# Kernel tuning notes

Hardware: AMD Instinct MI355X
Metric: run time of the kernel (lower is better)

The kernel has to match this reference:

```python
import jax, jax.numpy as jnp
import numpy as np
from jax import lax

N = 131072
E = 2097152
D = 128
B = 16
NC = 5
EPS = 1e-5


def setup_inputs() -> dict:
    key = jax.random.key(0)
    ks = jax.random.split(key, 32)
    inp = {
        'h': jax.random.normal(ks[0], (N, D), jnp.float32),
        'edge_w': jax.random.uniform(ks[1], (E,), jnp.float32),
        'src': jax.random.randint(ks[2], (E,), 0, N),
        'dst': jax.random.randint(ks[3], (E,), 0, N),
        'node_gid': jnp.sort(jax.random.randint(ks[4], (N,), 0, B)),
        'num_graphs': B,
    }
    s = 0.05
    inp['conv1_w'] = jax.random.normal(ks[5], (D, D, 3), jnp.float32) * s
    inp['conv1_b'] = jax.random.normal(ks[6], (D,), jnp.float32) * s
    inp['conv2_w'] = jax.random.normal(ks[7], (D, D, 3), jnp.float32) * s
    inp['conv2_b'] = jax.random.normal(ks[8], (D,), jnp.float32) * s
    inp['conv3_w'] = jax.random.normal(ks[9], (D, D, 3), jnp.float32) * s
    inp['conv3_b'] = jax.random.normal(ks[10], (D,), jnp.float32) * s
    inp['press_w'] = jax.random.normal(ks[11], (1, 3, 3), jnp.float32) * s
    inp['press_b'] = jax.random.normal(ks[12], (1,), jnp.float32) * s
    names = ['g11', 'g12', 'g13', 'g2', 'g3', 'g4']
    for i, nm in enumerate(names):
        inp[nm + '_w'] = jax.random.normal(ks[13 + 2 * i], (D, D), jnp.float32) * s
        inp[nm + '_b'] = jax.random.normal(ks[14 + 2 * i], (D,), jnp.float32) * s
    inp['bn_g'] = jnp.ones((D,), jnp.float32)
    inp['bn_b'] = jnp.zeros((D,), jnp.float32)
    inp['cls1_w'] = jax.random.normal(ks[25], (D, 3 * D), jnp.float32) * s
    inp['cls1_b'] = jax.random.normal(ks[26], (D,), jnp.float32) * s
    inp['cls2_w'] = jax.random.normal(ks[27], (NC, D), jnp.float32) * s
    inp['cls2_b'] = jax.random.normal(ks[28], (NC,), jnp.float32) * s
    return inp


def _conv1d_nodes(x, w, b, dil, pad):
    # x: [N, D] treated as a length-N 1D signal with D channels (as in original)
    y = lax.conv_general_dilated(x.T[None], w, window_strides=(1,),
                                 padding=[(pad, pad)], rhs_dilation=(dil,),
                                 dimension_numbers=('NCH', 'OIH', 'NCH'))
    return (y[0] + b[:, None]).T  # [N, D]


def _bn(x, g, b):
    mu = jnp.mean(x, axis=0)
    var = jnp.mean((x - mu) ** 2, axis=0)
    return (x - mu) * lax.rsqrt(var + EPS) * g + b


def _gconv(h, W, b, src, dst, ew, n):
    # DGL GraphConv norm='none': aggregate-first (in==out), msg = h[src]*ew, sum at dst, then @W + b
    msg = h[src] * ew[:, None]            # [E, D]
    agg = jax.ops.segment_sum(msg, dst, num_segments=n)
    return agg @ W + b


def reference(h, edge_w, src, dst, node_gid, num_graphs,
              conv1_w, conv1_b, conv2_w, conv2_b, conv3_w, conv3_b,
              press_w, press_b,
              g11_w, g11_b, g12_w, g12_b, g13_w, g13_b,
              g2_w, g2_b, g3_w, g3_b, g4_w, g4_b,
              bn_g, bn_b, cls1_w, cls1_b, cls2_w, cls2_b):
    n = h.shape[0]
    c1 = _conv1d_nodes(h, conv1_w, conv1_b, 1, 1)
    c2 = _conv1d_nodes(h, conv2_w, conv2_b, 2, 2)
    c3 = _conv1d_nodes(h, conv3_w, conv3_b, 3, 3)
    h01 = _bn(jax.nn.relu(c1) + c2, bn_g, bn_b)
    h02 = _bn(jax.nn.relu(c2) + c3, bn_g, bn_b)
    h03 = _bn(jax.nn.relu(c3) + c1, bn_g, bn_b)

    a1 = jax.nn.relu(_gconv(h01, g11_w, g11_b, src, dst, edge_w, n))
    a2 = jax.nn.relu(_gconv(h02, g12_w, g12_b, src, dst, edge_w, n))
    a3 = jax.nn.relu(_gconv(h03, g13_w, g13_b, src, dst, edge_w, n))
    stacked = jnp.stack([a1, a2, a3], axis=1)  # [N, 3, D]
    pressed = lax.conv_general_dilated(stacked, press_w, window_strides=(1,),
                                       padding=[(1, 1)],
                                       dimension_numbers=('NCH', 'OIH', 'NCH'))
    ac_h1 = pressed[:, 0, :] + press_b  # [N, D]
    ac_h1 = _bn(ac_h1, bn_g, bn_b)      # dropout is identity in eval

    ac_h2 = jax.nn.relu(_gconv(ac_h1, g2_w, g2_b, src, dst, edge_w, n))
    ac_h3 = jax.nn.relu(_gconv(ac_h2, g3_w, g3_b, src, dst, edge_w, n))
    ac_h4 = jax.nn.relu(_gconv(ac_h3, g4_w, g4_b, src, dst, edge_w, n))

    hg2 = jax.ops.segment_sum(ac_h2, node_gid, num_segments=num_graphs)
    hg3 = jax.ops.segment_sum(ac_h3, node_gid, num_segments=num_graphs)
    hg4 = jax.ops.segment_sum(ac_h4, node_gid, num_segments=num_graphs)
    hg = jnp.concatenate([hg2, hg3, hg4], axis=1)  # [B, 3D]
    out = (hg @ cls1_w.T + cls1_b) @ cls2_w.T + cls2_b  # [B, NC]
    return out
```

## Files before the change

kernel.cpp:

```cpp
#include <hip/hip_runtime.h>

#define NN 131072
#define NE 2097152

typedef unsigned short u16;
typedef unsigned int u32;
typedef __attribute__((ext_vector_type(8))) short bf16x8;
typedef __attribute__((ext_vector_type(4))) float f32x4;
typedef __attribute__((ext_vector_type(2))) float f32x2;

__device__ __forceinline__ float bf2f(u16 v) {
  unsigned u = ((unsigned)v) << 16;
  return __builtin_bit_cast(float, u);
}
__device__ __forceinline__ float blo(u32 v) {
  return __builtin_bit_cast(float, v << 16);
}
__device__ __forceinline__ float bhi(u32 v) {
  return __builtin_bit_cast(float, v & 0xffff0000u);
}
__device__ __forceinline__ u16 f2bf(float f) {
  unsigned u = __builtin_bit_cast(unsigned, f);
  unsigned r = (u + 0x7fffu + ((u >> 16) & 1u)) >> 16;
  return (u16)r;
}

#define WDQ 3.0518509475997192e-05f

#define H16_OFF 0ull
#define A_OFF 33554432ull
#define B_OFF 67108864ull
#define C_OFF 100663296ull
#define Z_OFF 134217728ull
#define RE_OFF 150994944ull
#define CSR_OFF 167772160ull
#define RP_OFF 184549376ull
#define DEG_OFF 185077760ull
#define SW_OFF 185602048ull
#define BS_OFF 186126336ull
#define SUMS_OFF 186130432ull
#define HG_OFF 186134528ull
#define WT16_OFF 186159104ull
#define WP16_OFF 186472448ull
#define CP_OFF 186681344ull
#define SV_OFF 186683392ull
#define SHV_OFF 186685440ull

__global__ void zerok(int* __restrict__ deg, float* __restrict__ sums,
                      float* __restrict__ hg) {
  int i = blockIdx.x * 256 + threadIdx.x;
  deg[i] = 0;
  if (i < 1024) sums[i] = 0.f;
  if (i < 6144) hg[i] = 0.f;
}

__global__ void h2bf(const float* __restrict__ h, u16* __restrict__ o) {
  int i = blockIdx.x * 256 + threadIdx.x;
  float4 v0 = *(const float4*)(h + (size_t)i * 8);
  float4 v1 = *(const float4*)(h + (size_t)i * 8 + 4);
  ushort4 a, b;
  a.x = f2bf(v0.x); a.y = f2bf(v0.y); a.z = f2bf(v0.z); a.w = f2bf(v0.w);
  b.x = f2bf(v1.x); b.y = f2bf(v1.y); b.z = f2bf(v1.z); b.w = f2bf(v1.w);
  *(ushort4*)(o + (size_t)i * 8) = a;
  *(ushort4*)(o + (size_t)i * 8 + 4) = b;
}

__global__ void prep_wT16(const float* __restrict__ w1, const float* __restrict__ w2,
                          const float* __restrict__ w3, u16* __restrict__ wT) {
  int e = blockIdx.x * 256 + threadIdx.x;
  if (e >= 3 * 3 * 128 * 128) return;
  int o = e & 127;
  int i = (e >> 7) & 127;
  int ct = e >> 14;
  int t = ct % 3, c = ct / 3;
  const float* w = (c == 0) ? w1 : (c == 1) ? w2 : w3;
  wT[(size_t)(c * 3 + t) * 17408 + o * 136 + i] = f2bf(w[(o * 128 + i) * 3 + t]);
}

__global__ void wprep16(const float* __restrict__ W, const float* __restrict__ sv,
                        u16* __restrict__ Wt) {
  int e = blockIdx.x * 256 + threadIdx.x;
  int o = e & 127, i = e >> 7;
  float s = sv ? sv[i] : 1.f;
  Wt[o * 136 + i] = f2bf(s * W[i * 128 + o]);
}

__global__ void cprep(const float* __restrict__ W, const float* __restrict__ shv,
                      float* __restrict__ cp) {
  int j = threadIdx.x;
  float a = 0.f;
  for (int i = 0; i < 128; ++i) a += shv[i] * W[i * 128 + j];
  cp[j] = a;
}

__global__ void bnparam(const float* __restrict__ sums, const float* __restrict__ g,
                        const float* __restrict__ b, float* __restrict__ sv,
                        float* __restrict__ shv, int tensor0) {
  int t = tensor0 + blockIdx.x;
  int o = threadIdx.x;
  float mu = sums[t * 256 + o] / (float)NN;
  float var = sums[t * 256 + 128 + o] / (float)NN - mu * mu;
  float s = g[o] * rsqrtf(var + 1e-5f);
  sv[t * 128 + o] = s;
  shv[t * 128 + o] = b[o] - mu * s;
}

template <int TAPS, int DIL, int OUT8>
__global__ __launch_bounds__(256, 4) void mfma_gemm(const u16* __restrict__ x,
                                                    const u16* __restrict__ wt,
                                                    u16* __restrict__ z) {
  __shared__ u16 sh[17408];
  int tid = threadIdx.x;
  int lane = tid & 63, wave = tid >> 6;
  int n0 = blockIdx.x * 128;
  int m = lane & 15, quad = lane >> 4;
  int koff = quad * 8;
  f32x4 acc[2][8];
#pragma unroll
  for (int a = 0; a < 2; ++a)
#pragma unroll
    for (int b = 0; b < 8; ++b) acc[a][b] = (f32x4){0.f, 0.f, 0.f, 0.f};
  int rbase = n0 + wave * 32 + m;

  for (int t = 0; t < TAPS; ++t) {
    if (TAPS > 1) __syncthreads();
    for (int idx = tid; idx < 2176; idx += 256)
      ((uint4*)sh)[idx] = ((const uint4*)(wt + (size_t)t * 17408))[idx];
    __syncthreads();
    const int shift = (TAPS == 3) ? (t - 1) * DIL : 0;
#pragma unroll
    for (int ks = 0; ks < 4; ++ks) {
      bf16x8 af[2];
#pragma unroll
      for (int rt = 0; rt < 2; ++rt) {
        int row = rbase + rt * 16 + shift;
        if (TAPS == 3) {
          int rc = min(max(row, 0), NN - 1);
          bf16x8 v = *(const bf16x8*)(x + (size_t)rc * 128 + ks * 32 + koff);
          bf16x8 zz = {};
          af[rt] = (row >= 0 && row < NN) ? v : zz;
        } else {
          af[rt] = *(const bf16x8*)(x + (size_t)row * 128 + ks * 32 + koff);
        }
      }
#pragma unroll
      for (int ct = 0; ct < 8; ++ct) {
        bf16x8 bf = *(const bf16x8*)(sh + (ct * 16 + m) * 136 + ks * 32 + koff);
        acc[0][ct] =
            __builtin_amdgcn_mfma_f32_16x16x32_bf16(af[0], bf, acc[0][ct], 0, 0, 0);
        acc[1][ct] =
            __builtin_amdgcn_mfma_f32_16x16x32_bf16(af[1], bf, acc[1][ct], 0, 0, 0);
      }
    }
  }
  __syncthreads();
#pragma unroll
  for (int rt = 0; rt < 2; ++rt)
#pragma unroll
    for (int ct = 0; ct < 8; ++ct)
#pragma unroll
      for (int r = 0; r < 4; ++r) {
        int rowl = wave * 32 + rt * 16 + quad * 4 + r;
        sh[rowl * 136 + ct * 16 + m] = f2bf(acc[rt][ct][r]);
      }
  __syncthreads();
  if (OUT8) {
    unsigned char* z8 = (unsigned char*)z;
#pragma unroll
    for (int it = 0; it < 8; ++it) {
      int q = tid + it * 256;
      int row = q >> 4, g = q & 15;
      uint4 v = *(const uint4*)(sh + row * 136 + g * 8);
      int w0 = __builtin_amdgcn_cvt_pk_fp8_f32(blo(v.x), bhi(v.x), 0, false);
      w0 = __builtin_amdgcn_cvt_pk_fp8_f32(blo(v.y), bhi(v.y), w0, true);
      int w1 = __builtin_amdgcn_cvt_pk_fp8_f32(blo(v.z), bhi(v.z), 0, false);
      w1 = __builtin_amdgcn_cvt_pk_fp8_f32(blo(v.w), bhi(v.w), w1, true);
      uint2 st;
      st.x = (u32)w0;
      st.y = (u32)w1;
      *(uint2*)(z8 + (size_t)(n0 + row) * 128 + g * 8) = st;
    }
  } else {
#pragma unroll
    for (int it = 0; it < 8; ++it) {
      int q = tid + it * 256;
      int row = q >> 4, g = q & 15;
      uint4 v = *(const uint4*)(sh + row * 136 + g * 8);
      *(uint4*)(z + (size_t)(n0 + row) * 128 + g * 8) = v;
    }
  }
}

__global__ __launch_bounds__(256) void combine(u16* __restrict__ A, u16* __restrict__ B,
                                               u16* __restrict__ C,
                                               const float* __restrict__ b1,
                                               const float* __restrict__ b2,
                                               const float* __restrict__ b3,
                                               float* __restrict__ sums) {
  __shared__ float red[2 * 128 * 6];
  int tid = threadIdx.x;
  int o = tid & 127, half = tid >> 7;
  int n0 = blockIdx.x * 32 + half * 16;
  float bb1 = b1[o], bb2 = b2[o], bb3 = b3[o];
  float s1 = 0, q1 = 0, s2 = 0, q2 = 0, s3 = 0, q3 = 0;
  for (int j = 0; j < 16; ++j) {
    size_t idx = (size_t)(n0 + j) * 128 + o;
    float c1 = bf2f(A[idx]) + bb1, c2 = bf2f(B[idx]) + bb2, c3 = bf2f(C[idx]) + bb3;
    float v1 = fmaxf(c1, 0.f) + c2;
    float v2 = fmaxf(c2, 0.f) + c3;
    float v3 = fmaxf(c3, 0.f) + c1;
    A[idx] = f2bf(v1);
    B[idx] = f2bf(v2);
    C[idx] = f2bf(v3);
    s1 += v1; q1 += v1 * v1;
    s2 += v2; q2 += v2 * v2;
    s3 += v3; q3 += v3 * v3;
  }
  int ri = (half * 128 + o) * 6;
  red[ri + 0] = s1; red[ri + 1] = q1; red[ri + 2] = s2;
  red[ri + 3] = q2; red[ri + 4] = s3; red[ri + 5] = q3;
  __syncthreads();
  if (half == 0) {
    int rj = (128 + o) * 6;
    atomicAdd(&sums[0 * 256 + o], s1 + red[rj + 0]);
    atomicAdd(&sums[0 * 256 + 128 + o], q1 + red[rj + 1]);
    atomicAdd(&sums[1 * 256 + o], s2 + red[rj + 2]);
    atomicAdd(&sums[1 * 256 + 128 + o], q2 + red[rj + 3]);
    atomicAdd(&sums[2 * 256 + o], s3 + red[rj + 4]);
    atomicAdd(&sums[2 * 256 + 128 + o], q3 + red[rj + 5]);
  }
}

__global__ void deg_rank_k(const int* __restrict__ dst, int* __restrict__ deg,
                           u16* __restrict__ re) {
  int e = blockIdx.x * 256 + threadIdx.x;
  if (e < NE) {
    int d = dst[e];
    int r = atomicAdd(&deg[d], 1);
    re[e] = (u16)r;
  }
}

__global__ void scan1(const int* __restrict__ deg, int* __restrict__ rp,
                      int* __restrict__ bs) {
  __shared__ int s[256];
  int t = threadIdx.x;
  int i = blockIdx.x * 256 + t;
  int v = deg[i];
  s[t] = v;
  for (int off = 1; off < 256; off <<= 1) {
    __syncthreads();
    int x = (t >= off) ? s[t - off] : 0;
    __syncthreads();
    s[t] += x;
  }
  rp[i] = s[t] - v;
  if (t == 255) bs[blockIdx.x] = s[255];
}

__global__ void scan2(int* __restrict__ bs) {
  __shared__ int s[512];
  int t = threadIdx.x;
  int v = bs[t];
  s[t] = v;
  for (int off = 1; off < 512; off <<= 1) {
    __syncthreads();
    int x = (t >= off) ? s[t - off] : 0;
    __syncthreads();
    s[t] += x;
  }
  bs[t] = s[t] - v;
}

__global__ void scan3(int* __restrict__ rp, const int* __restrict__ bs) {
  int i = blockIdx.x * 256 + threadIdx.x;
  rp[i] = rp[i] + bs[blockIdx.x];
  if (i == 0) rp[NN] = NE;
}

__global__ void csr_fill2(const int* __restrict__ src, const int* __restrict__ dst,
                          const float* __restrict__ ew, const int* __restrict__ rp,
                          const u16* __restrict__ re, u32* __restrict__ csrP) {
  int e = blockIdx.x * 256 + threadIdx.x;
  if (e < NE) {
    int d = dst[e];
    int p = rp[d] + (int)re[e];
    u32 q = (u32)(ew[e] * 32767.f + 0.5f);
    csrP[p] = (u32)src[e] | (q << 17);
  }
}

#define AB3 4
__global__ __launch_bounds__(256, 4) void agg3_press(
    const unsigned char* __restrict__ z1, const unsigned char* __restrict__ z2,
    const unsigned char* __restrict__ z3, const u32* __restrict__ csrP,
    const int* __restrict__ rp,
    const float* __restrict__ cp, const float* __restrict__ b1,
    const float* __restrict__ b2, const float* __restrict__ b3,
    const float* __restrict__ pw, const float* __restrict__ pb,
    u16* __restrict__ P, float* __restrict__ sums) {
  __shared__ u16 otile[4][16 * 128];
  __shared__ int ls_rp[4][17];
  int lane = threadIdx.x & 63, wave = threadIdx.x >> 6;
  int d0 = blockIdx.x * 64 + wave * 16;
  if (lane < 17) ls_rp[wave][lane] = rp[d0 + lane];
  float c1x = cp[lane * 2], c1y = cp[lane * 2 + 1];
  float c2x = cp[128 + lane * 2], c2y = cp[128 + lane * 2 + 1];
  float c3x = cp[256 + lane * 2], c3y = cp[256 + lane * 2 + 1];
  float b1x = b1[lane * 2], b1y = b1[lane * 2 + 1];
  float b2x = b2[lane * 2], b2y = b2[lane * 2 + 1];
  float b3x = b3[lane * 2], b3y = b3[lane * 2 + 1];
  float w10 = pw[0], w11 = pw[1], w12 = pw[2];
  float w20 = pw[3], w21 = pw[4], w22 = pw[5];
  float w30 = pw[6], w31 = pw[7], w32 = pw[8];
  float pbv = pb[0];
  __syncthreads();
  int s0 = __builtin_amdgcn_readfirstlane(ls_rp[wave][0]);
  int e0 = __builtin_amdgcn_readfirstlane(ls_rp[wave][16]);
  u32 vob = (u32)(lane * 2);
  float ax1 = 0.f, ay1 = 0.f, ax2 = 0.f, ay2 = 0.f, ax3 = 0.f, ay3 = 0.f;
  float wsum = 0.f;
  float sx = 0.f, qx = 0.f, sy = 0.f, qy = 0.f;
  int ld = 0;
  int nb = __builtin_amdgcn_readfirstlane(ls_rp[wave][1]);

  auto flush = [&]() {
    float swd = wsum;
    float a1x = fmaxf(ax1 + c1x * swd + b1x, 0.f);
    float a1y = fmaxf(ay1 + c1y * swd + b1y, 0.f);
    float a2x = fmaxf(ax2 + c2x * swd + b2x, 0.f);
    float a2y = fmaxf(ay2 + c2y * swd + b2y, 0.f);
    float a3x = fmaxf(ax3 + c3x * swd + b3x, 0.f);
    float a3y = fmaxf(ay3 + c3y * swd + b3y, 0.f);
    float l1 = __shfl_up(a1y, 1); if (lane == 0) l1 = 0.f;
    float l2 = __shfl_up(a2y, 1); if (lane == 0) l2 = 0.f;
    float l3 = __shfl_up(a3y, 1); if (lane == 0) l3 = 0.f;
    float r1 = __shfl_down(a1x, 1); if (lane == 63) r1 = 0.f;
    float r2 = __shfl_down(a2x, 1); if (lane == 63) r2 = 0.f;
    float r3 = __shfl_down(a3x, 1); if (lane == 63) r3 = 0.f;
    float ox = w10 * l1 + w11 * a1x + w12 * a1y + w20 * l2 + w21 * a2x +
               w22 * a2y + w30 * l3 + w31 * a3x + w32 * a3y + pbv;
    float oy = w10 * a1x + w11 * a1y + w12 * r1 + w20 * a2x + w21 * a2y +
               w22 * r2 + w30 * a3x + w31 * a3y + w32 * r3 + pbv;
    u32 pk2 = ((u32)f2bf(oy) << 16) | (u32)f2bf(ox);
    *(u32*)&otile[wave][ld * 128 + lane * 2] = pk2;
    sx += ox; qx += ox * ox;
    sy += oy; qy += oy * oy;
    ax1 = ay1 = ax2 = ay2 = ax3 = ay3 = 0.f;
    wsum = 0.f;
    ++ld;
    nb = __builtin_amdgcn_readfirstlane(ls_rp[wave][ld < 16 ? ld + 1 : 16]);
  };

  if (s0 < e0) {
    int e0m1 = e0 - 1;
    u32 pkA[AB3], pkB[AB3];
    u32 vaA[AB3], vbA[AB3], vcA[AB3], vaB[AB3], vbB[AB3], vcB[AB3];
    float wvA[AB3], wvB[AB3];

#define LOADPK3(PK, J0)                               \
  _Pragma("unroll") for (int k = 0; k < AB3; ++k) {   \
    int jc = (J0) + k;                                \
    jc = jc < e0 ? jc : e0m1;                         \
    PK[k] = csrP[jc];                                 \
  }
#define ISSUE3(VA, VB, VC, WV, PK)                    \
  _Pragma("unroll") for (int k = 0; k < AB3; ++k) {   \
    u32 p = PK[k];                                    \
    u32 off = ((p & 0x1FFFFu) << 7) | vob;            \
    VA[k] = *(const u16*)(z1 + off);                  \
    VB[k] = *(const u16*)(z2 + off);                  \
    VC[k] = *(const u16*)(z3 + off);                  \
    WV[k] = (float)(p >> 17) * WDQ;                   \
  }
#define CONS3(VA, VB, VC, WV, J0)                     \
  _Pragma("unroll") for (int k = 0; k < AB3; ++k) {   \
    int j = (J0) + k;                                 \
    if (j < e0) {                                     \
      while (j >= nb) flush();                        \
      float w = WV[k];                                \
      wsum += w;                                      \
      f32x2 d1 = __builtin_amdgcn_cvt_pk_f32_fp8((int)VA[k], false); \
      f32x2 d2 = __builtin_amdgcn_cvt_pk_f32_fp8((int)VB[k], false); \
      f32x2 d3 = __builtin_amdgcn_cvt_pk_f32_fp8((int)VC[k], false); \
      ax1 += d1.x * w; ay1 += d1.y * w;               \
      ax2 += d2.x * w; ay2 += d2.y * w;               \
      ax3 += d3.x * w; ay3 += d3.y * w;               \
    }                                                 \
  }

    LOADPK3(pkA, s0)
    ISSUE3(vaA, vbA, vcA, wvA, pkA)
    LOADPK3(pkA, s0 + AB3)
    int jb = s0;
    while (true) {
      LOADPK3(pkB, jb + 2 * AB3)
      if (jb + AB3 < e0) { ISSUE3(vaB, vbB, vcB, wvB, pkA) }
      CONS3(vaA, vbA, vcA, wvA, jb)
      if (jb + AB3 >= e0) break;
      LOADPK3(pkA, jb + 3 * AB3)
      if (jb + 2 * AB3 < e0) { ISSUE3(vaA, vbA, vcA, wvA, pkB) }
      CONS3(vaB, vbB, vcB, wvB, jb + AB3)
      if (jb + 2 * AB3 >= e0) break;
      jb += 2 * AB3;
    }
#undef LOADPK3
#undef ISSUE3
#undef CONS3
  }
  while (ld < 16) flush();

  {
    const u16* srcl = &otile[wave][0];
    u16* dstg = P + (size_t)d0 * 128;
#pragma unroll
    for (int i = 0; i < 4; ++i) {
      uint4 v = *(const uint4*)(srcl + i * 512 + lane * 8);
      *(uint4*)(dstg + i * 512 + lane * 8) = v;
    }
  }
  __syncthreads();
  float* red = (float*)&otile[0][0];
  int base = wave * 256 + lane * 4;
  red[base] = sx; red[base + 1] = qx; red[base + 2] = sy; red[base + 3] = qy;
  __syncthreads();
  int t = threadIdx.x;
  if (t < 64) {
    float s0_ = 0, q0_ = 0, s1_ = 0, q1_ = 0;
#pragma unroll
    for (int w = 0; w < 4; ++w) {
      int rb = w * 256 + t * 4;
      s0_ += red[rb]; q0_ += red[rb + 1]; s1_ += red[rb + 2]; q1_ += red[rb + 3];
    }
    atomicAdd(&sums[768 + t * 2], s0_);
    atomicAdd(&sums[768 + 128 + t * 2], q0_);
    atomicAdd(&sums[768 + t * 2 + 1], s1_);
    atomicAdd(&sums[768 + 128 + t * 2 + 1], q1_);
  }
}

#define AB2 8
__global__ __launch_bounds__(256, 4) void agg2(const unsigned char* __restrict__ z,
                                               const u32* __restrict__ csrP,
                                               const int* __restrict__ rp,
                                               const float* __restrict__ cvec,
                                               const float* __restrict__ bvec,
                                               u16* __restrict__ out,
                                               const int* __restrict__ gid,
                                               float* __restrict__ hg, int coloff) {
  __shared__ u16 otile[4][16 * 128];
  __shared__ int ls_rp[4][17];
  __shared__ int ls_gid[4][16];
  int lane = threadIdx.x & 63, wave = threadIdx.x >> 6;
  int d0 = blockIdx.x * 64 + wave * 16;
  if (lane < 17) ls_rp[wave][lane] = rp[d0 + lane];
  if (lane < 16) ls_gid[wave][lane] = gid[d0 + lane];
  float bx = bvec[lane * 2], by = bvec[lane * 2 + 1];
  float cx = cvec ? cvec[lane * 2] : 0.f;
  float cy = cvec ? cvec[lane * 2 + 1] : 0.f;
  __syncthreads();
  int s0 = __builtin_amdgcn_readfirstlane(ls_rp[wave][0]);
  int e0 = __builtin_amdgcn_readfirstlane(ls_rp[wave][16]);
  u32 vob = (u32)(lane * 2);
  float ax = 0.f, ay = 0.f, wsum = 0.f;
  int ld = 0;
  int nb = __builtin_amdgcn_readfirstlane(ls_rp[wave][1]);

  auto flush = [&]() {
    float rx = fmaxf(ax + cx * wsum + bx, 0.f);
    float ry = fmaxf(ay + cy * wsum + by, 0.f);
    u32 pk2 = ((u32)f2bf(ry) << 16) | (u32)f2bf(rx);
    *(u32*)&otile[wave][ld * 128 + lane * 2] = pk2;
    ax = 0.f;
    ay = 0.f;
    wsum = 0.f;
    ++ld;
    nb = __builtin_amdgcn_readfirstlane(ls_rp[wave][ld < 16 ? ld + 1 : 16]);
  };

  if (s0 < e0) {
    int e0m1 = e0 - 1;
    u32 pkA[AB2], pkB[AB2];
    u32 vaA[AB2], vaB[AB2];
    float wvA[AB2], wvB[AB2];

#define LOADPK1(PK, J0)                               \
  _Pragma("unroll") for (int k = 0; k < AB2; ++k) {   \
    int jc = (J0) + k;                                \
    jc = jc < e0 ? jc : e0m1;                         \
    PK[k] = csrP[jc];                                 \
  }
#define ISSUE1(VA, WV, PK)                            \
  _Pragma("unroll") for (int k = 0; k < AB2; ++k) {   \
    u32 p = PK[k];                                    \
    u32 off = ((p & 0x1FFFFu) << 7) | vob;            \
    VA[k] = *(const u16*)(z + off);                   \
    WV[k] = (float)(p >> 17) * WDQ;                   \
  }
#define CONS1(VA, WV, J0)                             \
  _Pragma("unroll") for (int k = 0; k < AB2; ++k) {   \
    int j = (J0) + k;                                 \
    if (j < e0) {                                     \
      while (j >= nb) flush();                        \
      float w = WV[k];                                \
      wsum += w;                                      \
      f32x2 d = __builtin_amdgcn_cvt_pk_f32_fp8((int)VA[k], false); \
      ax += d.x * w;                                  \
      ay += d.y * w;                                  \
    }                                                 \
  }

    LOADPK1(pkA, s0)
    ISSUE1(vaA, wvA, pkA)
    LOADPK1(pkA, s0 + AB2)
    int jb = s0;
    while (true) {
      LOADPK1(pkB, jb + 2 * AB2)
      if (jb + AB2 < e0) { ISSUE1(vaB, wvB, pkA) }
      CONS1(vaA, wvA, jb)
      if (jb + AB2 >= e0) break;
      LOADPK1(pkA, jb + 3 * AB2)
      if (jb + 2 * AB2 < e0) { ISSUE1(vaA, wvA, pkB) }
      CONS1(vaB, wvB, jb + AB2)
      if (jb + 2 * AB2 >= e0) break;
      jb += 2 * AB2;
    }
#undef LOADPK1
#undef ISSUE1
#undef CONS1
  }
  while (ld < 16) flush();

  {
    const u16* srcl = &otile[wave][0];
    u16* dstg = out + (size_t)d0 * 128;
#pragma unroll
    for (int i = 0; i < 4; ++i) {
      uint4 v = *(const uint4*)(srcl + i * 512 + lane * 8);
      *(uint4*)(dstg + i * 512 + lane * 8) = v;
    }
  }
  {
    float runx = 0.f, runy = 0.f;
    int curg = __builtin_amdgcn_readfirstlane(ls_gid[wave][0]);
    for (int r = 0; r < 16; ++r) {
      u32 v = *(const u32*)&otile[wave][r * 128 + lane * 2];
      float rx = blo(v), ry = bhi(v);
      int gn = __builtin_amdgcn_readfirstlane(ls_gid[wave][r]);
      if (gn != curg) {
        atomicAdd(&hg[curg * 384 + coloff + lane * 2], runx);
        atomicAdd(&hg[curg * 384 + coloff + lane * 2 + 1], runy);
        runx = 0.f;
        runy = 0.f;
        curg = gn;
      }
      runx += rx;
      runy += ry;
    }
    atomicAdd(&hg[curg * 384 + coloff + lane * 2], runx);
    atomicAdd(&hg[curg * 384 + coloff + lane * 2 + 1], runy);
  }
}

__global__ void classifier(const float* __restrict__ hg, const float* __restrict__ w1,
                           const float* __restrict__ b1, const float* __restrict__ w2,
                           const float* __restrict__ b2, float* __restrict__ out) {
  __shared__ float sh_hg[16 * 384];
  __shared__ float sh_z[16 * 128];
  int t = threadIdx.x;
  for (int u = t; u < 16 * 384; u += 256) sh_hg[u] = hg[u];
  __syncthreads();
  for (int u = 0; u < 8; ++u) {
    int idx = t + u * 256;
    int b = idx >> 7, o = idx & 127;
    float a = b1[o];
    for (int i = 0; i < 384; ++i) a += sh_hg[b * 384 + i] * w1[o * 384 + i];
    sh_z[b * 128 + o] = a;
  }
  __syncthreads();
  if (t < 80) {
    int b = t / 5, c = t % 5;
    float a = b2[c];
    for (int i = 0; i < 128; ++i) a += sh_z[b * 128 + i] * w2[c * 128 + i];
    out[b * 5 + c] = a;
  }
}

extern "C" void kernel_launch(void* const* d_in, const int* in_sizes, int n_in,
                              void* d_out, int out_size, void* d_ws, size_t ws_size,
                              hipStream_t stream) {
  const float* h = (const float*)d_in[0];
  const float* edge_w = (const float*)d_in[1];
  const int* src = (const int*)d_in[2];
  const int* dst = (const int*)d_in[3];
  const int* gid = (const int*)d_in[4];
  const float* c1w = (const float*)d_in[6];
  const float* c1b = (const float*)d_in[7];
  const float* c2w = (const float*)d_in[8];
  const float* c2b = (const float*)d_in[9];
  const float* c3w = (const float*)d_in[10];
  const float* c3b = (const float*)d_in[11];
  const float* pw = (const float*)d_in[12];
  const float* pb = (const float*)d_in[13];
  const float* g11w = (const float*)d_in[14];
  const float* g11b = (const float*)d_in[15];
  const float* g12w = (const float*)d_in[16];
  const float* g12b = (const float*)d_in[17];
  const float* g13w = (const float*)d_in[18];
  const float* g13b = (const float*)d_in[19];
  const float* g2w = (const float*)d_in[20];
  const float* g2b = (const float*)d_in[21];
  const float* g3w = (const float*)d_in[22];
  const float* g3b = (const float*)d_in[23];
  const float* g4w = (const float*)d_in[24];
  const float* g4b = (const float*)d_in[25];
  const float* bng = (const float*)d_in[26];
  const float* bnb = (const float*)d_in[27];
  const float* cl1w = (const float*)d_in[28];
  const float* cl1b = (const float*)d_in[29];
  const float* cl2w = (const float*)d_in[30];
  const float* cl2b = (const float*)d_in[31];

  char* ws = (char*)d_ws;
  u16* H16 = (u16*)(ws + H16_OFF);
  u16* A = (u16*)(ws + A_OFF);
  u16* B = (u16*)(ws + B_OFF);
  u16* C = (u16*)(ws + C_OFF);
  unsigned char* F1 = (unsigned char*)(ws + H16_OFF);
  unsigned char* F2 = (unsigned char*)(ws + H16_OFF + 16777216);
  unsigned char* F3 = (unsigned char*)(ws + Z_OFF);
  u16* re = (u16*)(ws + RE_OFF);
  u16* P = (u16*)(ws + A_OFF);
  u32* csrP = (u32*)(ws + CSR_OFF);
  int* rp = (int*)(ws + RP_OFF);
  int* deg = (int*)(ws + DEG_OFF);
  int* bs = (int*)(ws + BS_OFF);
  float* sums = (float*)(ws + SUMS_OFF);
  float* hg = (float*)(ws + HG_OFF);
  u16* wT16 = (u16*)(ws + WT16_OFF);
  u16* wP16 = (u16*)(ws + WP16_OFF);
  float* cp = (float*)(ws + CP_OFF);
  float* sv = (float*)(ws + SV_OFF);
  float* shv = (float*)(ws + SHV_OFF);
  float* outp = (float*)d_out;

  zerok<<<512, 256, 0, stream>>>(deg, sums, hg);
  h2bf<<<8192, 256, 0, stream>>>(h, H16);
  prep_wT16<<<1728, 256, 0, stream>>>(c1w, c2w, c3w, wT16);
  wprep16<<<64, 256, 0, stream>>>(g3w, (const float*)nullptr, wP16 + 4 * 17408);
  wprep16<<<64, 256, 0, stream>>>(g4w, (const float*)nullptr, wP16 + 5 * 17408);

  mfma_gemm<3, 1, 0><<<1024, 256, 0, stream>>>(H16, wT16 + 0 * 52224, A);
  mfma_gemm<3, 2, 0><<<1024, 256, 0, stream>>>(H16, wT16 + 1 * 52224, B);
  mfma_gemm<3, 3, 0><<<1024, 256, 0, stream>>>(H16, wT16 + 2 * 52224, C);
  combine<<<4096, 256, 0, stream>>>(A, B, C, c1b, c2b, c3b, sums);

  deg_rank_k<<<8192, 256, 0, stream>>>(dst, deg, re);
  scan1<<<512, 256, 0, stream>>>(deg, rp, bs);
  scan2<<<1, 512, 0, stream>>>(bs);
  scan3<<<512, 256, 0, stream>>>(rp, bs);
  csr_fill2<<<8192, 256, 0, stream>>>(src, dst, edge_w, rp, re, csrP);

  bnparam<<<3, 128, 0, stream>>>(sums, bng, bnb, sv, shv, 0);
  wprep16<<<64, 256, 0, stream>>>(g11w, sv + 0 * 128, wP16 + 0 * 17408);
  cprep<<<1, 128, 0, stream>>>(g11w, shv + 0 * 128, cp + 0 * 128);
  wprep16<<<64, 256, 0, stream>>>(g12w, sv + 1 * 128, wP16 + 1 * 17408);
  cprep<<<1, 128, 0, stream>>>(g12w, shv + 1 * 128, cp + 1 * 128);
  wprep16<<<64, 256, 0, stream>>>(g13w, sv + 2 * 128, wP16 + 2 * 17408);
  cprep<<<1, 128, 0, stream>>>(g13w, shv + 2 * 128, cp + 2 * 128);

  mfma_gemm<1, 0, 1><<<1024, 256, 0, stream>>>(A, wP16 + 0 * 17408, (u16*)F1);
  mfma_gemm<1, 0, 1><<<1024, 256, 0, stream>>>(B, wP16 + 1 * 17408, (u16*)F2);
  mfma_gemm<1, 0, 1><<<1024, 256, 0, stream>>>(C, wP16 + 2 * 17408, (u16*)F3);
  agg3_press<<<2048, 256, 0, stream>>>(F1, F2, F3, csrP, rp, cp, g11b, g12b,
                                       g13b, pw, pb, P, sums);

  bnparam<<<1, 128, 0, stream>>>(sums, bng, bnb, sv, shv, 3);
  wprep16<<<64, 256, 0, stream>>>(g2w, sv + 3 * 128, wP16 + 3 * 17408);
  cprep<<<1, 128, 0, stream>>>(g2w, shv + 3 * 128, cp + 3 * 128);

  mfma_gemm<1, 0, 1><<<1024, 256, 0, stream>>>(P, wP16 + 3 * 17408, (u16*)F1);
  agg2<<<2048, 256, 0, stream>>>(F1, csrP, rp, cp + 3 * 128, g2b, B, gid, hg, 0);
  mfma_gemm<1, 0, 1><<<1024, 256, 0, stream>>>(B, wP16 + 4 * 17408, (u16*)F1);
  agg2<<<2048, 256, 0, stream>>>(F1, csrP, rp, (const float*)nullptr, g3b, C, gid, hg, 128);
  mfma_gemm<1, 0, 1><<<1024, 256, 0, stream>>>(C, wP16 + 5 * 17408, (u16*)F1);
  agg2<<<2048, 256, 0, stream>>>(F1, csrP, rp, (const float*)nullptr, g4b, A, gid, hg, 256);

  classifier<<<1, 256, 0, stream>>>(hg, cl1w, cl1b, cl2w, cl2b, outp);
}
```

Baseline: 1.219 ms.

## Interleave two fp8 feature tables, fuse degree counting into h conversion, deepen gather batching

The first two fp8 feature outputs now go into one interleaved 256-byte-per-node table, so agg3_press fetches both branch values for a source node from the same row. This is meant to improve locality of the random edge gathers. The degree/rank atomic counting is folded into the bf16 conversion kernel, which removes one launch and its separate pass over dst. The gather batch sizes (AB3, AB2) are doubled to keep more loads in flight, at the cost of higher register pressure.

```diff
diff --git a/kernel.cpp b/kernel.cpp
--- a/kernel.cpp
+++ b/kernel.cpp
@@ -36,7 +36,6 @@
 #define CSR_OFF 167772160ull
 #define RP_OFF 184549376ull
 #define DEG_OFF 185077760ull
-#define SW_OFF 185602048ull
 #define BS_OFF 186126336ull
 #define SUMS_OFF 186130432ull
 #define HG_OFF 186134528ull
@@ -54,7 +53,9 @@
   if (i < 6144) hg[i] = 0.f;
 }
 
-__global__ void h2bf(const float* __restrict__ h, u16* __restrict__ o) {
+__global__ void h2bf_deg(const float* __restrict__ h, u16* __restrict__ o,
+                         const int* __restrict__ dst, int* __restrict__ deg,
+                         u16* __restrict__ re) {
   int i = blockIdx.x * 256 + threadIdx.x;
   float4 v0 = *(const float4*)(h + (size_t)i * 8);
   float4 v1 = *(const float4*)(h + (size_t)i * 8 + 4);
@@ -63,6 +64,9 @@
   b.x = f2bf(v1.x); b.y = f2bf(v1.y); b.z = f2bf(v1.z); b.w = f2bf(v1.w);
   *(ushort4*)(o + (size_t)i * 8) = a;
   *(ushort4*)(o + (size_t)i * 8 + 4) = b;
+  int d = dst[i];
+  int r = atomicAdd(&deg[d], 1);
+  re[i] = (u16)r;
 }
 
 __global__ void prep_wT16(const float* __restrict__ w1, const float* __restrict__ w2,
@@ -108,7 +112,7 @@
 template <int TAPS, int DIL, int OUT8>
 __global__ __launch_bounds__(256, 4) void mfma_gemm(const u16* __restrict__ x,
                                                     const u16* __restrict__ wt,
-                                                    u16* __restrict__ z) {
+                                                    u16* __restrict__ z, int zsb) {
   __shared__ u16 sh[17408];
   int tid = threadIdx.x;
   int lane = tid & 63, wave = tid >> 6;
@@ -178,7 +182,7 @@
       uint2 st;
       st.x = (u32)w0;
       st.y = (u32)w1;
-      *(uint2*)(z8 + (size_t)(n0 + row) * 128 + g * 8) = st;
+      *(uint2*)(z8 + (size_t)(n0 + row) * zsb + g * 8) = st;
     }
   } else {
 #pragma unroll
@@ -231,16 +235,6 @@
   }
 }
 
-__global__ void deg_rank_k(const int* __restrict__ dst, int* __restrict__ deg,
-                           u16* __restrict__ re) {
-  int e = blockIdx.x * 256 + threadIdx.x;
-  if (e < NE) {
-    int d = dst[e];
-    int r = atomicAdd(&deg[d], 1);
-    re[e] = (u16)r;
-  }
-}
-
 __global__ void scan1(const int* __restrict__ deg, int* __restrict__ rp,
                       int* __restrict__ bs) {
   __shared__ int s[256];
@@ -290,11 +284,10 @@
   }
 }
 
-#define AB3 4
+#define AB3 8
 __global__ __launch_bounds__(256, 4) void agg3_press(
-    const unsigned char* __restrict__ z1, const unsigned char* __restrict__ z2,
-    const unsigned char* __restrict__ z3, const u32* __restrict__ csrP,
-    const int* __restrict__ rp,
+    const unsigned char* __restrict__ z12, const unsigned char* __restrict__ z3,
+    const u32* __restrict__ csrP, const int* __restrict__ rp,
     const float* __restrict__ cp, const float* __restrict__ b1,
     const float* __restrict__ b2, const float* __restrict__ b3,
     const float* __restrict__ pw, const float* __restrict__ pb,
@@ -367,10 +360,12 @@
 #define ISSUE3(VA, VB, VC, WV, PK)                    \
   _Pragma("unroll") for (int k = 0; k < AB3; ++k) {   \
     u32 p = PK[k];                                    \
-    u32 off = ((p & 0x1FFFFu) << 7) | vob;            \
-    VA[k] = *(const u16*)(z1 + off);                  \
-    VB[k] = *(const u16*)(z2 + off);                  \
-    VC[k] = *(const u16*)(z3 + off);                  \
+    u32 sidx = p & 0x1FFFFu;                          \
+    u32 off12 = (sidx << 8) | vob;                    \
+    u32 off3 = (sidx << 7) | vob;                     \
+    VA[k] = *(const u16*)(z12 + off12);               \
+    VB[k] = *(const u16*)(z12 + off12 + 128);         \
+    VC[k] = *(const u16*)(z3 + off3);                 \
     WV[k] = (float)(p >> 17) * WDQ;                   \
   }
 #define CONS3(VA, VB, VC, WV, J0)                     \
@@ -439,7 +434,7 @@
   }
 }
 
-#define AB2 8
+#define AB2 16
 __global__ __launch_bounds__(256, 4) void agg2(const unsigned char* __restrict__ z,
                                                const u32* __restrict__ csrP,
                                                const int* __restrict__ rp,
@@ -626,9 +621,9 @@
   u16* A = (u16*)(ws + A_OFF);
   u16* B = (u16*)(ws + B_OFF);
   u16* C = (u16*)(ws + C_OFF);
-  unsigned char* F1 = (unsigned char*)(ws + H16_OFF);
-  unsigned char* F2 = (unsigned char*)(ws + H16_OFF + 16777216);
+  unsigned char* F12 = (unsigned char*)(ws + H16_OFF);
   unsigned char* F3 = (unsigned char*)(ws + Z_OFF);
+  unsigned char* FS2 = (unsigned char*)(ws + H16_OFF);
   u16* re = (u16*)(ws + RE_OFF);
   u16* P = (u16*)(ws + A_OFF);
   u32* csrP = (u32*)(ws + CSR_OFF);
@@ -645,17 +640,16 @@
   float* outp = (float*)d_out;
 
   zerok<<<512, 256, 0, stream>>>(deg, sums, hg);
-  h2bf<<<8192, 256, 0, stream>>>(h, H16);
+  h2bf_deg<<<8192, 256, 0, stream>>>(h, H16, dst, deg, re);
   prep_wT16<<<1728, 256, 0, stream>>>(c1w, c2w, c3w, wT16);
   wprep16<<<64, 256, 0, stream>>>(g3w, (const float*)nullptr, wP16 + 4 * 17408);
   wprep16<<<64, 256, 0, stream>>>(g4w, (const float*)nullptr, wP16 + 5 * 17408);
 
-  mfma_gemm<3, 1, 0><<<1024, 256, 0, stream>>>(H16, wT16 + 0 * 52224, A);
-  mfma_gemm<3, 2, 0><<<1024, 256, 0, stream>>>(H16, wT16 + 1 * 52224, B);
-  mfma_gemm<3, 3, 0><<<1024, 256, 0, stream>>>(H16, wT16 + 2 * 52224, C);
+  mfma_gemm<3, 1, 0><<<1024, 256, 0, stream>>>(H16, wT16 + 0 * 52224, A, 0);
+  mfma_gemm<3, 2, 0><<<1024, 256, 0, stream>>>(H16, wT16 + 1 * 52224, B, 0);
+  mfma_gemm<3, 3, 0><<<1024, 256, 0, stream>>>(H16, wT16 + 2 * 52224, C, 0);
   combine<<<4096, 256, 0, stream>>>(A, B, C, c1b, c2b, c3b, sums);
 
-  deg_rank_k<<<8192, 256, 0, stream>>>(dst, deg, re);
   scan1<<<512, 256, 0, stream>>>(deg, rp, bs);
   scan2<<<1, 512, 0, stream>>>(bs);
   scan3<<<512, 256, 0, stream>>>(rp, bs);
@@ -669,22 +663,22 @@
   wprep16<<<64, 256, 0, stream>>>(g13w, sv + 2 * 128, wP16 + 2 * 17408);
   cprep<<<1, 128, 0, stream>>>(g13w, shv + 2 * 128, cp + 2 * 128);
 
-  mfma_gemm<1, 0, 1><<<1024, 256, 0, stream>>>(A, wP16 + 0 * 17408, (u16*)F1);
-  mfma_gemm<1, 0, 1><<<1024, 256, 0, stream>>>(B, wP16 + 1 * 17408, (u16*)F2);
-  mfma_gemm<1, 0, 1><<<1024, 256, 0, stream>>>(C, wP16 + 2 * 17408, (u16*)F3);
-  agg3_press<<<2048, 256, 0, stream>>>(F1, F2, F3, csrP, rp, cp, g11b, g12b,
+  mfma_gemm<1, 0, 1><<<1024, 256, 0, stream>>>(A, wP16 + 0 * 17408, (u16*)F12, 256);
+  mfma_gemm<1, 0, 1><<<1024, 256, 0, stream>>>(B, wP16 + 1 * 17408, (u16*)(F12 + 128), 256);
+  mfma_gemm<1, 0, 1><<<1024, 256, 0, stream>>>(C, wP16 + 2 * 17408, (u16*)F3, 128);
+  agg3_press<<<2048, 256, 0, stream>>>(F12, F3, csrP, rp, cp, g11b, g12b,
                                        g13b, pw, pb, P, sums);
 
   bnparam<<<1, 128, 0, stream>>>(sums, bng, bnb, sv, shv, 3);
   wprep16<<<64, 256, 0, stream>>>(g2w, sv + 3 * 128, wP16 + 3 * 17408);
   cprep<<<1, 128, 0, stream>>>(g2w, shv + 3 * 128, cp + 3 * 128);
 
-  mfma_gemm<1, 0, 1><<<1024, 256, 0, stream>>>(P, wP16 + 3 * 17408, (u16*)F1);
-  agg2<<<2048, 256, 0, stream>>>(F1, csrP, rp, cp + 3 * 128, g2b, B, gid, hg, 0);
-  mfma_gemm<1, 0, 1><<<1024, 256, 0, stream>>>(B, wP16 + 4 * 17408, (u16*)F1);
-  agg2<<<2048, 256, 0, stream>>>(F1, csrP, rp, (const float*)nullptr, g3b, C, gid, hg, 128);
-  mfma_gemm<1, 0, 1><<<1024, 256, 0, stream>>>(C, wP16 + 5 * 17408, (u16*)F1);
-  agg2<<<2048, 256, 0, stream>>>(F1, csrP, rp, (const float*)nullptr, g4b, A, gid, hg, 256);
+  mfma_gemm<1, 0, 1><<<1024, 256, 0, stream>>>(P, wP16 + 3 * 17408, (u16*)FS2, 128);
+  agg2<<<2048, 256, 0, stream>>>(FS2, csrP, rp, cp + 3 * 128, g2b, B, gid, hg, 0);
+  mfma_gemm<1, 0, 1><<<1024, 256, 0, stream>>>(B, wP16 + 4 * 17408, (u16*)FS2, 128);
+  agg2<<<2048, 256, 0, stream>>>(FS2, csrP, rp, (const float*)nullptr, g3b, C, gid, hg, 128);
+  mfma_gemm<1, 0, 1><<<1024, 256, 0, stream>>>(C, wP16 + 5 * 17408, (u16*)FS2, 128);
+  agg2<<<2048, 256, 0, stream>>>(FS2, csrP, rp, (const float*)nullptr, g4b, A, gid, hg, 256);
 
   classifier<<<1, 256, 0, stream>>>(hg, cl1w, cl1b, cl2w, cl2b, outp);
 }
```

New measurement: 1.273 ms. +4.5%, slower.
